# Kernel optimization log

Measured on AMD Instinct MI355X. Metric: run time of the kernel, lower is better.

The kernel has to match this reference:

```python
import jax, jax.numpy as jnp
import numpy as np

B, N, C, H, P, DP = 2, 512, 384, 12, 4, 128
CH = C // H
SCALE = CH ** -0.5
EPS = 1e-5


def setup_inputs() -> dict:
    key = jax.random.key(0)
    ks = jax.random.split(key, 16)
    w = lambda k, i, o: jax.random.normal(k, (i, o), jnp.float32) * 0.02
    inp = {
        'single': jax.random.normal(ks[0], (B, N, C), jnp.float32),
        'pair': jax.random.normal(ks[1], (B, N, N, DP), jnp.float32),
        'rot': jax.random.normal(ks[2], (B, N, 3, 3), jnp.float32),
        'trans': jax.random.normal(ks[3], (B, N, 3), jnp.float32),
        'mask': jnp.ones((B, N), jnp.float32),
        'Wq': w(ks[4], C, C), 'bq': jnp.zeros((C,)),
        'Wk': w(ks[5], C, C), 'bk': jnp.zeros((C,)),
        'Wv': w(ks[6], C, C), 'bv': jnp.zeros((C,)),
        'Wpb': w(ks[7], DP, H), 'bpb': jnp.zeros((H,)),
        'Wqp': w(ks[8], C, H * P * 3), 'bqp': jnp.zeros((H * P * 3,)),
        'Wkp': w(ks[9], C, H * P * 3), 'bkp': jnp.zeros((H * P * 3,)),
        'Wvp': w(ks[10], C, H * P * 3), 'bvp': jnp.zeros((H * P * 3,)),
        'Wo': w(ks[11], C, C), 'bo': jnp.zeros((C,)),
        'Wpo': w(ks[12], H * P * 3, C), 'bpo': jnp.zeros((C,)),
        'ln_g': jnp.ones((C,)), 'ln_b': jnp.zeros((C,)),
    }
    return inp


def _to_global(pts, rot, trans):
    # pts: [B,N,H,P,3], rot: [B,N,3,3], trans: [B,N,3]
    return jnp.einsum('bnhpd,bnde->bnhpe', pts, rot) + trans[:, :, None, None, :]


def reference(single, pair, rot, trans, mask,
              Wq, bq, Wk, bk, Wv, bv, Wpb, bpb,
              Wqp, bqp, Wkp, bkp, Wvp, bvp,
              Wo, bo, Wpo, bpo, ln_g, ln_b):
    q = (single @ Wq + bq).reshape(B, N, H, CH)
    k = (single @ Wk + bk).reshape(B, N, H, CH)
    v = (single @ Wv + bv).reshape(B, N, H, CH)
    pair_bias = jnp.transpose(pair @ Wpb + bpb, (0, 3, 1, 2))  # [B,H,N,N]

    q_pts = (single @ Wqp + bqp).reshape(B, N, H, P, 3)
    k_pts = (single @ Wkp + bkp).reshape(B, N, H, P, 3)
    qg = _to_global(q_pts, rot, trans)
    kg = _to_global(k_pts, rot, trans)

    q2 = jnp.sum(qg * qg, axis=(3, 4))  # [B,N,H]
    k2 = jnp.sum(kg * kg, axis=(3, 4))
    qk = jnp.einsum('bnhpd,bmhpd->bhnm', qg, kg)
    q2h = jnp.transpose(q2, (0, 2, 1))  # [B,H,N]
    k2h = jnp.transpose(k2, (0, 2, 1))
    point_logits = -0.5 * (q2h[..., :, None] + k2h[..., None, :] - 2.0 * qk) * SCALE

    scalar_logits = jnp.einsum('bnhc,bmhc->bhnm', q, k) * SCALE
    logits = scalar_logits + pair_bias + point_logits

    mask2d = mask[:, None, :, None] * mask[:, None, None, :]  # [B,1,N,N]
    logits = jnp.where(mask2d == 0, -1e9, logits)
    attn = jax.nn.softmax(logits, axis=-1)

    weighted_scalar = jnp.einsum('bhnm,bmhc->bnhc', attn, v).reshape(B, N, C)

    v_pts = (single @ Wvp + bvp).reshape(B, N, H, P, 3)
    vg = _to_global(v_pts, rot, trans)
    weighted_points = jnp.einsum('bhnm,bmhpd->bnhpd', attn, vg).reshape(B, N, H * P * 3)

    point_proj = weighted_points @ Wpo + bpo
    out = (weighted_scalar + point_proj) @ Wo + bo

    x = single + out
    mu = jnp.mean(x, axis=-1, keepdims=True)
    var = jnp.mean((x - mu) ** 2, axis=-1, keepdims=True)
    return (x - mu) * jax.lax.rsqrt(var + EPS) * ln_g + ln_b
```

## Files before the change

kernel.cpp:

```cpp
#include <hip/hip_runtime.h>
#include <hip/hip_bf16.h>

#define Bb   2
#define Nn   512
#define Cc   384
#define Hh   12
#define BN   1024
#define NC1  1584
#define CT1  99
#define SCALE 0.17677669529663687f

typedef __attribute__((ext_vector_type(8))) short short8;
typedef __attribute__((ext_vector_type(4))) float f32x4;

__device__ __forceinline__ unsigned short f2bf(float f){
  union { float f; unsigned u; } v; v.f = f;
  unsigned u = v.u;
  unsigned r = u + 0x7fffu + ((u >> 16) & 1u);
  return (unsigned short)(r >> 16);
}
__device__ __forceinline__ float bf_lo(unsigned u){ union{unsigned u; float f;} v; v.u = u << 16; return v.f; }
__device__ __forceinline__ float bf_hi(unsigned u){ union{unsigned u; float f;} v; v.u = u & 0xffff0000u; return v.f; }
__device__ __forceinline__ unsigned pack2(float a, float b){
  return (unsigned)f2bf(a) | ((unsigned)f2bf(b) << 16);
}

__device__ __forceinline__ void bias_job16(const float* __restrict__ pair,
    const float* __restrict__ Wpb, const float* __restrict__ bpb,
    unsigned short* __restrict__ biasf, int jd, int tid, unsigned short* lds)
{
  int l = tid & 63, w = tid >> 6;
  int b = jd >> 9, r9 = jd & 511;
  int it = r9 >> 4, jt = r9 & 15;
  int i0 = it << 4, j0 = jt << 5;
  int kb = (l >> 4) << 3;
  int h = l & 15;
  short8 bf[4];
#pragma unroll
  for (int t = 0; t < 4; ++t){
#pragma unroll
    for (int j = 0; j < 8; ++j){
      int k = t * 32 + kb + j;
      float v = (h < 12) ? Wpb[k * 12 + h] : 0.f;
      bf[t][j] = (short)f2bf(v);
    }
  }
  float bb = (h < 12) ? bpb[h] : 0.f;

  for (int s = 0; s < 8; ++s){
    int tile = s * 4 + w;
    int iloc = tile >> 1, jh = tile & 1;
    long m = ((long)(b * 512 + i0 + iloc)) * 512 + j0 + jh * 16 + (l & 15);
    const float* pr = pair + m * 128 + kb;
    f32x4 acc = {0,0,0,0};
#pragma unroll
    for (int t = 0; t < 4; ++t){
      float4 x0 = *(const float4*)(pr + t * 32);
      float4 x1 = *(const float4*)(pr + t * 32 + 4);
      short8 a;
      a[0] = (short)f2bf(x0.x); a[1] = (short)f2bf(x0.y);
      a[2] = (short)f2bf(x0.z); a[3] = (short)f2bf(x0.w);
      a[4] = (short)f2bf(x1.x); a[5] = (short)f2bf(x1.y);
      a[6] = (short)f2bf(x1.z); a[7] = (short)f2bf(x1.w);
      acc = __builtin_amdgcn_mfma_f32_16x16x32_bf16(a, bf[t], acc, 0, 0, 0);
    }
    if (h < 12){
      int jloc = jh * 16 + ((l >> 4) << 2);
      unsigned short* dst = lds + (h * 17 + iloc) * 36 + jloc;
      uint2 wv; wv.x = pack2(acc[0] + bb, acc[1] + bb); wv.y = pack2(acc[2] + bb, acc[3] + bb);
      *(uint2*)dst = wv;
    }
  }
  __syncthreads();

  for (int e = tid; e < 12 * 2 * 64; e += 256){
    int run = e >> 6, idx = e & 63;
    int h2 = run >> 1, f = run & 1;
    int g2 = idx >> 4, q = idx & 15;
    const unsigned short* src = lds + (h2 * 17 + q) * 36 + f * 16 + g2 * 4;
    uint2 v = *(const uint2*)src;
    long base = ((((long)(b * 12 + h2) * 16 + jt) * 32 + it) * 2 + f) * 64 + idx;
    *(uint2*)(biasf + base * 4) = v;
  }
}

__global__ __launch_bounds__(256) void k1_prep_bias(
    const float* __restrict__ single,
    const float* __restrict__ Wq, const float* __restrict__ Wk, const float* __restrict__ Wv,
    const float* __restrict__ Wqp, const float* __restrict__ Wkp, const float* __restrict__ Wvp,
    const float* __restrict__ bq, const float* __restrict__ bk, const float* __restrict__ bv,
    const float* __restrict__ bqp, const float* __restrict__ bkp, const float* __restrict__ bvp,
    const float* __restrict__ Wpo, const float* __restrict__ Wo,
    const float* __restrict__ pair, const float* __restrict__ Wpb, const float* __restrict__ bpb,
    unsigned short* __restrict__ sbf, unsigned short* __restrict__ wcat, float* __restrict__ bcat,
    unsigned short* __restrict__ wpof, unsigned short* __restrict__ wof,
    unsigned short* __restrict__ wppad, unsigned short* __restrict__ biasf)
{
  __shared__ __align__(16) unsigned short blds[16 * 17 * 36];
  int bid = blockIdx.x, tid = threadIdx.x;
  if (bid >= 256){ bias_job16(pair, Wpb, bpb, biasf, bid - 256, tid, blds); return; }

  const int n0 = BN * Cc;
  const int n1 = 12 * CT1 * 512;
  const int n4 = NC1;
  const int n5 = 61440;
  const int n6 = 147456;
  const int n7 = BN * 16;
  const int total = n0 + n1 + n4 + n5 + n6 + n7;
  for (int i = bid * 256 + tid; i < total; i += 256 * 256){
    int e = i;
    if (e < n0){ sbf[e] = f2bf(single[e]); continue; }
    e -= n0;
    if (e < n1){
      int j8 = e & 7, l = (e >> 3) & 63, ctt = e >> 9;
      int ct = ctt % CT1, t = ctt / CT1;
      int k = t * 32 + ((l >> 4) << 3) + j8;
      int col = (ct << 4) + (l & 15);
      float v;
      if (col < 1152){
        const float* W = (col < 384) ? Wq : (col < 768 ? Wk : Wv);
        v = W[k * 384 + (col % 384)];
      } else {
        int c2 = col - 1152;
        const float* W = (c2 < 144) ? Wqp : (c2 < 288 ? Wkp : Wvp);
        v = W[k * 144 + (c2 % 144)];
      }
      wcat[e] = f2bf(v); continue;
    }
    e -= n1;
    if (e < n4){
      int col = e; float v;
      if (col < 1152){
        const float* bb = (col < 384) ? bq : (col < 768 ? bk : bv);
        v = bb[col % 384];
      } else {
        int c2 = col - 1152;
        const float* bb = (c2 < 144) ? bqp : (c2 < 288 ? bkp : bvp);
        v = bb[c2 % 144];
      }
      bcat[col] = v; continue;
    }
    e -= n4;
    if (e < n5){
      int j8 = e & 7, l = (e >> 3) & 63, ctt = e >> 9;
      int ct = ctt % 24, t = ctt / 24;
      int k = t * 32 + ((l >> 4) << 3) + j8;
      int col = (ct << 4) + (l & 15);
      wpof[e] = (k < 144) ? f2bf(Wpo[k * 384 + col]) : (unsigned short)0;
      continue;
    }
    e -= n5;
    if (e < n6){
      int j8 = e & 7, l = (e >> 3) & 63, ctt = e >> 9;
      int ct = ctt % 24, t = ctt / 24;
      int k = t * 32 + ((l >> 4) << 3) + j8;
      int col = (ct << 4) + (l & 15);
      wof[e] = f2bf(Wo[k * 384 + col]);
      continue;
    }
    e -= n6;
    { int row = e >> 4, c = e & 15; wppad[row * 160 + 144 + c] = 0; }
  }
}

__global__ __launch_bounds__(256) void k2_proj_bias(
    const unsigned short* __restrict__ sbf, const unsigned short* __restrict__ wcat,
    const float* __restrict__ bcat, float* __restrict__ proj,
    const float* __restrict__ pair, const float* __restrict__ Wpb, const float* __restrict__ bpb,
    unsigned short* __restrict__ biasf)
{
  __shared__ __align__(16) unsigned short blds[16 * 17 * 36];
  int bid = blockIdx.x, tid = threadIdx.x;
  if (bid >= 528){ bias_job16(pair, Wpb, bpb, biasf, 192 + (bid - 528), tid, blds); return; }

  int l = tid & 63, w = tid >> 6;
  int bx = bid & 15, by = bid >> 4;
  int m0 = bx * 64 + w * 16;
  const unsigned short* Ap = sbf + (long)(m0 + (l & 15)) * Cc + ((l >> 4) << 3);
  int ct0 = by * 3;
  f32x4 acc0 = {0,0,0,0}, acc1 = {0,0,0,0}, acc2 = {0,0,0,0};
  for (int t = 0; t < 12; ++t){
    short8 a = *(const short8*)(Ap + t * 32);
    const unsigned short* wp_ = wcat + ((long)(t * CT1 + ct0) * 64 + l) * 8;
    short8 b0 = *(const short8*)(wp_);
    short8 b1 = *(const short8*)(wp_ + 512);
    short8 b2 = *(const short8*)(wp_ + 1024);
    acc0 = __builtin_amdgcn_mfma_f32_16x16x32_bf16(a, b0, acc0, 0, 0, 0);
    acc1 = __builtin_amdgcn_mfma_f32_16x16x32_bf16(a, b1, acc1, 0, 0, 0);
    acc2 = __builtin_amdgcn_mfma_f32_16x16x32_bf16(a, b2, acc2, 0, 0, 0);
  }
  int rbase = m0 + ((l >> 4) << 2);
  int cb = by * 48 + (l & 15);
#pragma unroll
  for (int c = 0; c < 3; ++c){
    f32x4 ac = (c == 0) ? acc0 : (c == 1 ? acc1 : acc2);
    int col = cb + c * 16;
    float bb = bcat[col];
#pragma unroll
    for (int r = 0; r < 4; ++r)
      proj[(long)(rbase + r) * NC1 + col] = ac[r] + bb;
  }
}

__global__ __launch_bounds__(256) void k3_pack_bias(
    const float* __restrict__ proj, const float* __restrict__ rot,
    const float* __restrict__ trans, const float* __restrict__ mask,
    unsigned short* __restrict__ qf, unsigned short* __restrict__ kf,
    unsigned short* __restrict__ vf, float* __restrict__ q2h, float* __restrict__ k2h,
    const float* __restrict__ pair, const float* __restrict__ Wpb, const float* __restrict__ bpb,
    unsigned short* __restrict__ biasf)
{
  __shared__ __align__(16) unsigned char smem3[23168];
  int bid = blockIdx.x, tid = threadIdx.x;
  if (bid >= 384){
    bias_job16(pair, Wpb, bpb, biasf, 576 + (bid - 384), tid, (unsigned short*)smem3);
    return;
  }

  float* scal = (float*)smem3;
  float* praw = scal + 3072;
  float* pg   = praw + 1152;
  float* rots = pg + 1152;
  float* trs  = rots + 288;
  float* msk  = trs + 96;

  int jid = bid;
  int b = jid / 192, rem = jid % 192;
  int h = rem >> 4, rt = rem & 15;
  int j0 = rt * 32;
  int bn0 = b * 512 + j0;
  int bh = b * 12 + h;

  for (int idx = tid; idx < 3072; idx += 256){
    int a = idx >> 10, row = (idx >> 5) & 31, c = idx & 31;
    scal[idx] = proj[(long)(bn0 + row) * NC1 + a * 384 + h * 32 + c];
  }
  for (int idx = tid; idx < 1152; idx += 256){
    int a = idx / 384, rr = idx % 384, row = rr / 12, pe = rr % 12;
    praw[idx] = proj[(long)(bn0 + row) * NC1 + 1152 + a * 144 + h * 12 + pe];
  }
  for (int idx = tid; idx < 288; idx += 256) rots[idx] = rot[(long)bn0 * 9 + idx];
  for (int idx = tid; idx < 96; idx += 256)  trs[idx] = trans[(long)bn0 * 3 + idx];
  for (int idx = tid; idx < 32; idx += 256)  msk[idx] = mask[bn0 + idx];
  __syncthreads();

  for (int idx = tid; idx < 1152; idx += 256){
    int a = idx / 384, rr = idx % 384, row = rr / 12, pe = rr % 12;
    int p = pe / 3, ee = pe % 3;
    pg[idx] = praw[a * 384 + row * 12 + p * 3] * rots[row * 9 + ee]
            + praw[a * 384 + row * 12 + p * 3 + 1] * rots[row * 9 + 3 + ee]
            + praw[a * 384 + row * 12 + p * 3 + 2] * rots[row * 9 + 6 + ee] + trs[row * 3 + ee];
  }
  __syncthreads();

  for (int idx = tid; idx < 64; idx += 256){
    int a = idx >> 5, row = idx & 31;
    float s2 = 0.f;
#pragma unroll
    for (int pe = 0; pe < 12; ++pe){ float g = pg[a * 384 + row * 12 + pe]; s2 += g * g; }
    float mv = msk[row];
    float rres = -0.5f * SCALE * s2 + (mv != 0.f ? 0.f : -2e9f);
    (a ? k2h : q2h)[(long)bh * 512 + j0 + row] = rres;
  }

  for (int idx = tid; idx < 2048; idx += 256){
    int a = idx >> 10, r = idx & 1023;
    int jjp = r & 3, l = (r >> 2) & 63, ks = (r >> 8) & 1, sub = r >> 9;
    int row = sub * 16 + (l & 15);
    int kk = ks * 32 + ((l >> 4) << 3) + jjp * 2;
    int k1 = kk + 1;
    float v0 = (kk < 32) ? scal[a * 1024 + row * 32 + kk] : (kk < 44 ? pg[a * 384 + row * 12 + kk - 32] : 0.f);
    float v1 = (k1 < 32) ? scal[a * 1024 + row * 32 + k1] : (k1 < 44 ? pg[a * 384 + row * 12 + k1 - 32] : 0.f);
    if (a == 0){ v0 *= SCALE; v1 *= SCALE; }
    unsigned* dst = (unsigned*)(a ? kf : qf);
    dst[((((long)bh * 32 + rt * 2 + sub) * 2 + ks) * 64 + l) * 4 + jjp] = pack2(v0, v1);
  }

  for (int idx = tid; idx < 768; idx += 256){
    int jjp = idx & 3, l = (idx >> 2) & 63, cf = idx >> 8;
    int c = cf * 16 + (l & 15);
    int j = ((l >> 4) << 3) + jjp * 2;
    float v0 = (c < 32) ? scal[2048 + j * 32 + c]       : (c < 44 ? pg[768 + j * 12 + (c - 32)]       : 0.f);
    float v1 = (c < 32) ? scal[2048 + (j + 1) * 32 + c] : (c < 44 ? pg[768 + (j + 1) * 12 + (c - 32)] : 0.f);
    ((unsigned*)vf)[(((long)bh * 16 + rt) * 3 + cf) * 256 + l * 4 + jjp] = pack2(v0, v1);
  }
}

__global__ __launch_bounds__(256) void attn2_kernel(
    const unsigned short* __restrict__ qf, const unsigned short* __restrict__ kf,
    const unsigned short* __restrict__ vf, const unsigned short* __restrict__ biasf,
    const float* __restrict__ q2h, const float* __restrict__ k2h,
    float* __restrict__ wsout, unsigned short* __restrict__ wpout)
{
  __shared__ unsigned short pls[4][16][40];
  __shared__ float oW[4][3][64][4];
  __shared__ float mW[4][16], lsW[4][16];
  __shared__ float fW[4][16], linvS[16];

  int l = threadIdx.x & 63, w = threadIdx.x >> 6;
  int qt = blockIdx.x, h = blockIdx.y, b = blockIdx.z;
  int bh = b * 12 + h;
  int g = l >> 4, q_ = l & 15;

  const short8* qp = (const short8*)(qf + (((long)(bh * 32 + qt) * 2) * 64 + l) * 8);
  short8 qA = qp[0], qB = qp[64];
  float cq = q2h[(long)bh * 512 + qt * 16 + q_];

  float m = -1e30f, ls = 0.f;
  f32x4 o0 = {0,0,0,0}, o1 = {0,0,0,0}, o2 = {0,0,0,0};
  const f32x4 z4 = {0,0,0,0};

#pragma unroll
  for (int ji = 0; ji < 4; ++ji){
    int jt = w * 4 + ji;
    const short8* kp = (const short8*)(kf + (((long)(bh * 32 + jt * 2) * 2) * 64 + l) * 8);
    short8 k00 = kp[0], k01 = kp[64], k10 = kp[128], k11 = kp[192];
    f32x4 s0 = __builtin_amdgcn_mfma_f32_16x16x32_bf16(k00, qA, z4, 0, 0, 0);
    s0 = __builtin_amdgcn_mfma_f32_16x16x32_bf16(k01, qB, s0, 0, 0, 0);
    f32x4 s1 = __builtin_amdgcn_mfma_f32_16x16x32_bf16(k10, qA, z4, 0, 0, 0);
    s1 = __builtin_amdgcn_mfma_f32_16x16x32_bf16(k11, qB, s1, 0, 0, 0);

    const uint2* bp = (const uint2*)(biasf + ((((long)(bh * 16 + jt) * 32 + qt) * 2) * 64) * 4);
    uint2 bb0 = bp[l], bb1 = bp[64 + l];
    const float4* k2p = (const float4*)(k2h + (long)bh * 512 + jt * 32);
    float4 ck0 = k2p[g], ck1 = k2p[4 + g];

    s0[0] += bf_lo(bb0.x) + cq + ck0.x;
    s0[1] += bf_hi(bb0.x) + cq + ck0.y;
    s0[2] += bf_lo(bb0.y) + cq + ck0.z;
    s0[3] += bf_hi(bb0.y) + cq + ck0.w;
    s1[0] += bf_lo(bb1.x) + cq + ck1.x;
    s1[1] += bf_hi(bb1.x) + cq + ck1.y;
    s1[2] += bf_lo(bb1.y) + cq + ck1.z;
    s1[3] += bf_hi(bb1.y) + cq + ck1.w;

    float tm = fmaxf(fmaxf(fmaxf(s0[0], s0[1]), fmaxf(s0[2], s0[3])),
                     fmaxf(fmaxf(s1[0], s1[1]), fmaxf(s1[2], s1[3])));
    tm = fmaxf(tm, __shfl_xor(tm, 16));
    tm = fmaxf(tm, __shfl_xor(tm, 32));
    float mn = fmaxf(m, tm);
    float alpha = __expf(m - mn);
    f32x4 p0, p1;
    float ts = 0.f;
#pragma unroll
    for (int r = 0; r < 4; ++r){ p0[r] = __expf(s0[r] - mn); ts += p0[r]; }
#pragma unroll
    for (int r = 0; r < 4; ++r){ p1[r] = __expf(s1[r] - mn); ts += p1[r]; }
    ts += __shfl_xor(ts, 16);
    ts += __shfl_xor(ts, 32);
    ls = ls * alpha + ts; m = mn;

    f32x4 av;
#pragma unroll
    for (int r = 0; r < 4; ++r) av[r] = __shfl(alpha, g * 4 + r);
#pragma unroll
    for (int r = 0; r < 4; ++r){ o0[r] *= av[r]; o1[r] *= av[r]; o2[r] *= av[r]; }

    uint2 w0; w0.x = pack2(p0[0], p0[1]); w0.y = pack2(p0[2], p0[3]);
    uint2 w1; w1.x = pack2(p1[0], p1[1]); w1.y = pack2(p1[2], p1[3]);
    *(uint2*)&pls[w][q_][g * 4]      = w0;
    *(uint2*)&pls[w][q_][16 + g * 4] = w1;
    short8 pa = *(const short8*)&pls[w][q_][g * 8];

    const short8* vp = (const short8*)(vf + (((long)(bh * 16 + jt) * 3) * 64 + l) * 8);
    short8 v0 = vp[0], v1 = vp[64], v2 = vp[128];
    o0 = __builtin_amdgcn_mfma_f32_16x16x32_bf16(pa, v0, o0, 0, 0, 0);
    o1 = __builtin_amdgcn_mfma_f32_16x16x32_bf16(pa, v1, o1, 0, 0, 0);
    o2 = __builtin_amdgcn_mfma_f32_16x16x32_bf16(pa, v2, o2, 0, 0, 0);
  }

  if (g == 0){ mW[w][q_] = m; lsW[w][q_] = ls; }
  *(f32x4*)&oW[w][0][l][0] = o0;
  *(f32x4*)&oW[w][1][l][0] = o1;
  *(f32x4*)&oW[w][2][l][0] = o2;
  __syncthreads();

  if (w == 0){
    float M = fmaxf(fmaxf(mW[0][q_], mW[1][q_]), fmaxf(mW[2][q_], mW[3][q_]));
    float f = __expf(mW[g][q_] - M);
    fW[g][q_] = f;
    float lf = lsW[g][q_] * f;
    lf += __shfl_xor(lf, 16);
    lf += __shfl_xor(lf, 32);
    if (g == 0) linvS[q_] = 1.f / lf;
  }
  __syncthreads();

  if (w < 3){
    float fr[4][4], li[4];
#pragma unroll
    for (int r = 0; r < 4; ++r){
      int q = g * 4 + r;
      li[r] = linvS[q];
#pragma unroll
      for (int vw = 0; vw < 4; ++vw) fr[vw][r] = fW[vw][q];
    }
    f32x4 sum = {0,0,0,0};
#pragma unroll
    for (int vw = 0; vw < 4; ++vw){
      f32x4 ov = *(const f32x4*)&oW[vw][w][l][0];
#pragma unroll
      for (int r = 0; r < 4; ++r) sum[r] += ov[r] * fr[vw][r];
    }
#pragma unroll
    for (int r = 0; r < 4; ++r){
      long bn = (long)b * 512 + qt * 16 + g * 4 + r;
      float val = sum[r] * li[r];
      if (w == 0)      wsout[bn * 384 + h * 32 + q_] = val;
      else if (w == 1) wsout[bn * 384 + h * 32 + 16 + q_] = val;
      else if (q_ < 12) wpout[bn * 160 + h * 12 + q_] = f2bf(val);
    }
  }
}

__global__ __launch_bounds__(256) void tail_kernel(
    const unsigned short* __restrict__ wpbuf, const unsigned short* __restrict__ wpof,
    const float* __restrict__ bpo, const float* __restrict__ wso,
    const unsigned short* __restrict__ wof, const float* __restrict__ bo,
    const float* __restrict__ single, const float* __restrict__ ln_g,
    const float* __restrict__ ln_b, float* __restrict__ out)
{
  __shared__ unsigned short t1s[16][392];
  __shared__ float redS[4][16], redQ[4][16];
  int l = threadIdx.x & 63, w = threadIdx.x >> 6;
  int m0 = blockIdx.x * 16;
  int rb = (l >> 4) << 2;
  int arow = m0 + (l & 15);

  {
    short8 awp[5];
    const unsigned short* Ap = wpbuf + (long)arow * 160 + ((l >> 4) << 3);
#pragma unroll
    for (int t = 0; t < 5; ++t) awp[t] = *(const short8*)(Ap + t * 32);
#pragma unroll
    for (int c6 = 0; c6 < 6; ++c6){
      int ct = w * 6 + c6;
      f32x4 acc = {0,0,0,0};
#pragma unroll
      for (int t = 0; t < 5; ++t){
        short8 bfr = *(const short8*)(wpof + ((long)(t * 24 + ct) * 64 + l) * 8);
        acc = __builtin_amdgcn_mfma_f32_16x16x32_bf16(awp[t], bfr, acc, 0, 0, 0);
      }
      int col = ct * 16 + (l & 15);
      float bb = bpo[col];
#pragma unroll
      for (int r = 0; r < 4; ++r){
        float v = acc[r] + bb + wso[(long)(m0 + rb + r) * 384 + col];
        t1s[rb + r][col] = f2bf(v);
      }
    }
  }
  __syncthreads();

  short8 a2[12];
  {
    int lr = l & 15;
#pragma unroll
    for (int t = 0; t < 12; ++t)
      a2[t] = *(const short8*)&t1s[lr][t * 32 + ((l >> 4) << 3)];
  }
  f32x4 xa[6];
  float s1[4] = {0,0,0,0}, s2[4] = {0,0,0,0};
#pragma unroll
  for (int c6 = 0; c6 < 6; ++c6){
    int ct = w * 6 + c6;
    f32x4 acc = {0,0,0,0};
#pragma unroll
    for (int t = 0; t < 12; ++t){
      short8 bfr = *(const short8*)(wof + ((long)(t * 24 + ct) * 64 + l) * 8);
      acc = __builtin_amdgcn_mfma_f32_16x16x32_bf16(a2[t], bfr, acc, 0, 0, 0);
    }
    int col = ct * 16 + (l & 15);
    float bb = bo[col];
#pragma unroll
    for (int r = 0; r < 4; ++r){
      float v = acc[r] + bb + single[(long)(m0 + rb + r) * 384 + col];
      acc[r] = v; s1[r] += v; s2[r] += v * v;
    }
    xa[c6] = acc;
  }
#pragma unroll
  for (int off = 1; off < 16; off <<= 1){
#pragma unroll
    for (int r = 0; r < 4; ++r){
      s1[r] += __shfl_xor(s1[r], off);
      s2[r] += __shfl_xor(s2[r], off);
    }
  }
  if ((l & 15) == 0){
#pragma unroll
    for (int r = 0; r < 4; ++r){ redS[w][rb + r] = s1[r]; redQ[w][rb + r] = s2[r]; }
  }
  __syncthreads();
  float mu[4], inv[4];
#pragma unroll
  for (int r = 0; r < 4; ++r){
    float ts = redS[0][rb + r] + redS[1][rb + r] + redS[2][rb + r] + redS[3][rb + r];
    float tq = redQ[0][rb + r] + redQ[1][rb + r] + redQ[2][rb + r] + redQ[3][rb + r];
    mu[r] = ts * (1.f / 384.f);
    float var = tq * (1.f / 384.f) - mu[r] * mu[r];
    inv[r] = rsqrtf(var + 1e-5f);
  }
#pragma unroll
  for (int c6 = 0; c6 < 6; ++c6){
    int ct = w * 6 + c6;
    int col = ct * 16 + (l & 15);
    float g = ln_g[col], bt = ln_b[col];
#pragma unroll
    for (int r = 0; r < 4; ++r)
      out[(long)(m0 + rb + r) * 384 + col] = (xa[c6][r] - mu[r]) * inv[r] * g + bt;
  }
}

extern "C" void kernel_launch(void* const* d_in, const int* in_sizes, int n_in,
                              void* d_out, int out_size, void* d_ws, size_t ws_size,
                              hipStream_t stream)
{
  const float* single = (const float*)d_in[0];
  const float* pair   = (const float*)d_in[1];
  const float* rot    = (const float*)d_in[2];
  const float* trans  = (const float*)d_in[3];
  const float* mask   = (const float*)d_in[4];
  const float* Wq  = (const float*)d_in[5];  const float* bq  = (const float*)d_in[6];
  const float* Wk  = (const float*)d_in[7];  const float* bk  = (const float*)d_in[8];
  const float* Wv  = (const float*)d_in[9];  const float* bv  = (const float*)d_in[10];
  const float* Wpb = (const float*)d_in[11]; const float* bpb = (const float*)d_in[12];
  const float* Wqp = (const float*)d_in[13]; const float* bqp = (const float*)d_in[14];
  const float* Wkp = (const float*)d_in[15]; const float* bkp = (const float*)d_in[16];
  const float* Wvp = (const float*)d_in[17]; const float* bvp = (const float*)d_in[18];
  const float* Wo  = (const float*)d_in[19]; const float* bo  = (const float*)d_in[20];
  const float* Wpo = (const float*)d_in[21]; const float* bpo = (const float*)d_in[22];
  const float* ln_g = (const float*)d_in[23]; const float* ln_b = (const float*)d_in[24];

  char* wsb = (char*)d_ws;
  size_t off = 0;
  auto alloc = [&](size_t bytes) -> void* {
    void* p = wsb + off; off += (bytes + 255) & ~(size_t)255; return p;
  };
  unsigned short* sbf  = (unsigned short*)alloc((size_t)BN * Cc * 2);
  unsigned short* wcat = (unsigned short*)alloc((size_t)12 * CT1 * 512 * 2);
  unsigned short* wpof = (unsigned short*)alloc((size_t)5 * 24 * 512 * 2);
  unsigned short* wof  = (unsigned short*)alloc((size_t)12 * 24 * 512 * 2);
  float* bcat  = (float*)alloc(NC1 * 4);
  float* proj  = (float*)alloc((size_t)BN * NC1 * 4);
  unsigned short* biasf = (unsigned short*)alloc((size_t)Bb * Hh * Nn * Nn * 2);
  unsigned short* qfragb = (unsigned short*)alloc((size_t)786432 * 2);
  unsigned short* kfragb = (unsigned short*)alloc((size_t)786432 * 2);
  unsigned short* vfragb = (unsigned short*)alloc((size_t)589824 * 2);
  float* q2hb  = (float*)alloc((size_t)12288 * 4);
  float* k2hb  = (float*)alloc((size_t)12288 * 4);
  float* wso   = (float*)alloc((size_t)BN * 384 * 4);
  unsigned short* wpbuf = (unsigned short*)alloc((size_t)BN * 160 * 2);
  if (off > ws_size) return;

  k1_prep_bias<<<256 + 192, 256, 0, stream>>>(
      single, Wq, Wk, Wv, Wqp, Wkp, Wvp, bq, bk, bv, bqp, bkp, bvp, Wpo, Wo,
      pair, Wpb, bpb, sbf, wcat, bcat, wpof, wof, wpbuf, biasf);
  k2_proj_bias<<<528 + 384, 256, 0, stream>>>(
      sbf, wcat, bcat, proj, pair, Wpb, bpb, biasf);
  k3_pack_bias<<<384 + 448, 256, 0, stream>>>(
      proj, rot, trans, mask, qfragb, kfragb, vfragb, q2hb, k2hb,
      pair, Wpb, bpb, biasf);
  attn2_kernel<<<dim3(32, 12, 2), 256, 0, stream>>>(qfragb, kfragb, vfragb, biasf,
                                                    q2hb, k2hb, wso, wpbuf);
  tail_kernel<<<64, 256, 0, stream>>>(wpbuf, wpof, bpo, wso, wof, bo,
                                      single, ln_g, ln_b, (float*)d_out);
}
```

Measured before the change: 96.12 us.

## Move all pair-bias jobs into the first kernel and unroll the bias loop

The pair-bias projection work was previously split across three kernels (k1, k2, k3) as extra blocks piggybacking on the projection and packing kernels. It is now done entirely by k1, which launches 1024 bias blocks, while k2 and k3 run only their own work. The bias inner loop is also unrolled by 2 to raise memory-level parallelism. This makes the bandwidth-heavy pair read one large phase instead of overlapping it with the small projection and packing kernels, which may reduce co-scheduling benefits but improves load balance and lowers LDS use in k2 and k3.

Result: slower. 105.5 us (+9.7%).

```diff
diff --git a/kernel.cpp b/kernel.cpp
--- a/kernel.cpp
+++ b/kernel.cpp
@@ -47,6 +47,7 @@
   }
   float bb = (h < 12) ? bpb[h] : 0.f;
 
+#pragma unroll 2
   for (int s = 0; s < 8; ++s){
     int tile = s * 4 + w;
     int iloc = tile >> 1, jh = tile & 1;
@@ -163,16 +164,11 @@
   }
 }
 
-__global__ __launch_bounds__(256) void k2_proj_bias(
+__global__ __launch_bounds__(256) void k2_proj(
     const unsigned short* __restrict__ sbf, const unsigned short* __restrict__ wcat,
-    const float* __restrict__ bcat, float* __restrict__ proj,
-    const float* __restrict__ pair, const float* __restrict__ Wpb, const float* __restrict__ bpb,
-    unsigned short* __restrict__ biasf)
-{
-  __shared__ __align__(16) unsigned short blds[16 * 17 * 36];
+    const float* __restrict__ bcat, float* __restrict__ proj)
+{
   int bid = blockIdx.x, tid = threadIdx.x;
-  if (bid >= 528){ bias_job16(pair, Wpb, bpb, biasf, 192 + (bid - 528), tid, blds); return; }
-
   int l = tid & 63, w = tid >> 6;
   int bx = bid & 15, by = bid >> 4;
   int m0 = bx * 64 + w * 16;
@@ -202,22 +198,16 @@
   }
 }
 
-__global__ __launch_bounds__(256) void k3_pack_bias(
+__global__ __launch_bounds__(256) void k3_pack(
     const float* __restrict__ proj, const float* __restrict__ rot,
     const float* __restrict__ trans, const float* __restrict__ mask,
     unsigned short* __restrict__ qf, unsigned short* __restrict__ kf,
-    unsigned short* __restrict__ vf, float* __restrict__ q2h, float* __restrict__ k2h,
-    const float* __restrict__ pair, const float* __restrict__ Wpb, const float* __restrict__ bpb,
-    unsigned short* __restrict__ biasf)
-{
-  __shared__ __align__(16) unsigned char smem3[23168];
+    unsigned short* __restrict__ vf, float* __restrict__ q2h, float* __restrict__ k2h)
+{
+  __shared__ float smemf[5792];
   int bid = blockIdx.x, tid = threadIdx.x;
-  if (bid >= 384){
-    bias_job16(pair, Wpb, bpb, biasf, 576 + (bid - 384), tid, (unsigned short*)smem3);
-    return;
-  }
-
-  float* scal = (float*)smem3;
+
+  float* scal = smemf;
   float* praw = scal + 3072;
   float* pg   = praw + 1152;
   float* rots = pg + 1152;
@@ -553,14 +543,12 @@
   unsigned short* wpbuf = (unsigned short*)alloc((size_t)BN * 160 * 2);
   if (off > ws_size) return;
 
-  k1_prep_bias<<<256 + 192, 256, 0, stream>>>(
+  k1_prep_bias<<<256 + 1024, 256, 0, stream>>>(
       single, Wq, Wk, Wv, Wqp, Wkp, Wvp, bq, bk, bv, bqp, bkp, bvp, Wpo, Wo,
       pair, Wpb, bpb, sbf, wcat, bcat, wpof, wof, wpbuf, biasf);
-  k2_proj_bias<<<528 + 384, 256, 0, stream>>>(
-      sbf, wcat, bcat, proj, pair, Wpb, bpb, biasf);
-  k3_pack_bias<<<384 + 448, 256, 0, stream>>>(
-      proj, rot, trans, mask, qfragb, kfragb, vfragb, q2hb, k2hb,
-      pair, Wpb, bpb, biasf);
+  k2_proj<<<528, 256, 0, stream>>>(sbf, wcat, bcat, proj);
+  k3_pack<<<384, 256, 0, stream>>>(proj, rot, trans, mask,
+                                   qfragb, kfragb, vfragb, q2hb, k2hb);
   attn2_kernel<<<dim3(32, 12, 2), 256, 0, stream>>>(qfragb, kfragb, vfragb, biasf,
                                                     q2hb, k2hb, wso, wpbuf);
   tail_kernel<<<64, 256, 0, stream>>>(wpbuf, wpof, bpo, wso, wof, bo,
```

## Fuse tail projection and layernorm into attention via last-block atomic counter

Applied to the files above, without the earlier changes.

The separate tail kernel is removed. Its output projection, residual add and layernorm now run inside the attention kernel, done by whichever of the 12 head blocks for a (batch, query tile) finishes last, found with an atomic counter and thread fences. The counter is reset in the first prep kernel. Bias fragments for all four key tiles are also prefetched into registers before the main loop. This saves one kernel launch and its tail latency, but adds more LDS and register pressure to the attention kernel and serialises the tail work onto the last-arriving blocks.

Result: slower. 169.3 us (+76.1%).

```diff
diff --git a/kernel.cpp b/kernel.cpp
--- a/kernel.cpp
+++ b/kernel.cpp
@@ -94,11 +94,14 @@
     const float* __restrict__ pair, const float* __restrict__ Wpb, const float* __restrict__ bpb,
     unsigned short* __restrict__ sbf, unsigned short* __restrict__ wcat, float* __restrict__ bcat,
     unsigned short* __restrict__ wpof, unsigned short* __restrict__ wof,
-    unsigned short* __restrict__ wppad, unsigned short* __restrict__ biasf)
+    unsigned short* __restrict__ wppad, unsigned short* __restrict__ biasf,
+    unsigned* __restrict__ cnt)
 {
   __shared__ __align__(16) unsigned short blds[16 * 17 * 36];
   int bid = blockIdx.x, tid = threadIdx.x;
   if (bid >= 256){ bias_job16(pair, Wpb, bpb, biasf, bid - 256, tid, blds); return; }
+
+  if (bid == 0 && tid < 64) cnt[tid] = 0;
 
   const int n0 = BN * Cc;
   const int n1 = 12 * CT1 * 512;
@@ -290,17 +293,34 @@
     const unsigned short* __restrict__ qf, const unsigned short* __restrict__ kf,
     const unsigned short* __restrict__ vf, const unsigned short* __restrict__ biasf,
     const float* __restrict__ q2h, const float* __restrict__ k2h,
-    float* __restrict__ wsout, unsigned short* __restrict__ wpout)
+    float* __restrict__ wsout, unsigned short* __restrict__ wpout,
+    const unsigned short* __restrict__ wpof, const float* __restrict__ bpo,
+    const unsigned short* __restrict__ wof, const float* __restrict__ bo,
+    const float* __restrict__ single, const float* __restrict__ ln_g,
+    const float* __restrict__ ln_b, float* __restrict__ out,
+    unsigned* __restrict__ cnt)
 {
   __shared__ unsigned short pls[4][16][40];
   __shared__ float oW[4][3][64][4];
   __shared__ float mW[4][16], lsW[4][16];
   __shared__ float fW[4][16], linvS[16];
+  __shared__ unsigned short t1s[16][392];
+  __shared__ float redS[4][16], redQ[4][16];
+  __shared__ int lastflag;
 
   int l = threadIdx.x & 63, w = threadIdx.x >> 6;
   int qt = blockIdx.x, h = blockIdx.y, b = blockIdx.z;
   int bh = b * 12 + h;
   int g = l >> 4, q_ = l & 15;
+
+  uint2 bpre[4][2];
+#pragma unroll
+  for (int ji = 0; ji < 4; ++ji){
+    int jt = w * 4 + ji;
+    const uint2* bp = (const uint2*)(biasf + ((((long)(bh * 16 + jt) * 32 + qt) * 2) * 64) * 4);
+    bpre[ji][0] = bp[l];
+    bpre[ji][1] = bp[64 + l];
+  }
 
   const short8* qp = (const short8*)(qf + (((long)(bh * 32 + qt) * 2) * 64 + l) * 8);
   short8 qA = qp[0], qB = qp[64];
@@ -320,8 +340,7 @@
     f32x4 s1 = __builtin_amdgcn_mfma_f32_16x16x32_bf16(k10, qA, z4, 0, 0, 0);
     s1 = __builtin_amdgcn_mfma_f32_16x16x32_bf16(k11, qB, s1, 0, 0, 0);
 
-    const uint2* bp = (const uint2*)(biasf + ((((long)(bh * 16 + jt) * 32 + qt) * 2) * 64) * 4);
-    uint2 bb0 = bp[l], bb1 = bp[64 + l];
+    uint2 bb0 = bpre[ji][0], bb1 = bpre[ji][1];
     const float4* k2p = (const float4*)(k2h + (long)bh * 512 + jt * 32);
     float4 ck0 = k2p[g], ck1 = k2p[4 + g];
 
@@ -411,25 +430,23 @@
       else if (q_ < 12) wpout[bn * 160 + h * 12 + q_] = f2bf(val);
     }
   }
-}
-
-__global__ __launch_bounds__(256) void tail_kernel(
-    const unsigned short* __restrict__ wpbuf, const unsigned short* __restrict__ wpof,
-    const float* __restrict__ bpo, const float* __restrict__ wso,
-    const unsigned short* __restrict__ wof, const float* __restrict__ bo,
-    const float* __restrict__ single, const float* __restrict__ ln_g,
-    const float* __restrict__ ln_b, float* __restrict__ out)
-{
-  __shared__ unsigned short t1s[16][392];
-  __shared__ float redS[4][16], redQ[4][16];
-  int l = threadIdx.x & 63, w = threadIdx.x >> 6;
-  int m0 = blockIdx.x * 16;
+
+  __threadfence();
+  __syncthreads();
+  if (threadIdx.x == 0){
+    unsigned old = atomicAdd(&cnt[b * 32 + qt], 1u);
+    lastflag = (old == 11u);
+  }
+  __syncthreads();
+  if (!lastflag) return;
+  __threadfence();
+
+  int m0t = b * 512 + qt * 16;
   int rb = (l >> 4) << 2;
-  int arow = m0 + (l & 15);
-
+  int arow = m0t + (l & 15);
   {
     short8 awp[5];
-    const unsigned short* Ap = wpbuf + (long)arow * 160 + ((l >> 4) << 3);
+    const unsigned short* Ap = wpout + (long)arow * 160 + ((l >> 4) << 3);
 #pragma unroll
     for (int t = 0; t < 5; ++t) awp[t] = *(const short8*)(Ap + t * 32);
 #pragma unroll
@@ -445,7 +462,7 @@
       float bb = bpo[col];
 #pragma unroll
       for (int r = 0; r < 4; ++r){
-        float v = acc[r] + bb + wso[(long)(m0 + rb + r) * 384 + col];
+        float v = acc[r] + bb + wsout[(long)(m0t + rb + r) * 384 + col];
         t1s[rb + r][col] = f2bf(v);
       }
     }
@@ -460,7 +477,7 @@
       a2[t] = *(const short8*)&t1s[lr][t * 32 + ((l >> 4) << 3)];
   }
   f32x4 xa[6];
-  float s1[4] = {0,0,0,0}, s2[4] = {0,0,0,0};
+  float s1a[4] = {0,0,0,0}, s2a[4] = {0,0,0,0};
 #pragma unroll
   for (int c6 = 0; c6 < 6; ++c6){
     int ct = w * 6 + c6;
@@ -474,8 +491,8 @@
     float bb = bo[col];
 #pragma unroll
     for (int r = 0; r < 4; ++r){
-      float v = acc[r] + bb + single[(long)(m0 + rb + r) * 384 + col];
-      acc[r] = v; s1[r] += v; s2[r] += v * v;
+      float v = acc[r] + bb + single[(long)(m0t + rb + r) * 384 + col];
+      acc[r] = v; s1a[r] += v; s2a[r] += v * v;
     }
     xa[c6] = acc;
   }
@@ -483,13 +500,13 @@
   for (int off = 1; off < 16; off <<= 1){
 #pragma unroll
     for (int r = 0; r < 4; ++r){
-      s1[r] += __shfl_xor(s1[r], off);
-      s2[r] += __shfl_xor(s2[r], off);
+      s1a[r] += __shfl_xor(s1a[r], off);
+      s2a[r] += __shfl_xor(s2a[r], off);
     }
   }
   if ((l & 15) == 0){
 #pragma unroll
-    for (int r = 0; r < 4; ++r){ redS[w][rb + r] = s1[r]; redQ[w][rb + r] = s2[r]; }
+    for (int r = 0; r < 4; ++r){ redS[w][rb + r] = s1a[r]; redQ[w][rb + r] = s2a[r]; }
   }
   __syncthreads();
   float mu[4], inv[4];
@@ -505,10 +522,10 @@
   for (int c6 = 0; c6 < 6; ++c6){
     int ct = w * 6 + c6;
     int col = ct * 16 + (l & 15);
-    float g = ln_g[col], bt = ln_b[col];
+    float gg = ln_g[col], bt = ln_b[col];
 #pragma unroll
     for (int r = 0; r < 4; ++r)
-      out[(long)(m0 + rb + r) * 384 + col] = (xa[c6][r] - mu[r]) * inv[r] * g + bt;
+      out[(long)(m0t + rb + r) * 384 + col] = (xa[c6][r] - mu[r]) * inv[r] * gg + bt;
   }
 }
 
@@ -551,18 +568,18 @@
   float* k2hb  = (float*)alloc((size_t)12288 * 4);
   float* wso   = (float*)alloc((size_t)BN * 384 * 4);
   unsigned short* wpbuf = (unsigned short*)alloc((size_t)BN * 160 * 2);
+  unsigned* cnt = (unsigned*)alloc(64 * 4);
   if (off > ws_size) return;
 
   k1_prep_bias<<<256 + 192, 256, 0, stream>>>(
       single, Wq, Wk, Wv, Wqp, Wkp, Wvp, bq, bk, bv, bqp, bkp, bvp, Wpo, Wo,
-      pair, Wpb, bpb, sbf, wcat, bcat, wpof, wof, wpbuf, biasf);
+      pair, Wpb, bpb, sbf, wcat, bcat, wpof, wof, wpbuf, biasf, cnt);
   k2_proj_bias<<<528 + 384, 256, 0, stream>>>(
       sbf, wcat, bcat, proj, pair, Wpb, bpb, biasf);
   k3_pack_bias<<<384 + 448, 256, 0, stream>>>(
       proj, rot, trans, mask, qfragb, kfragb, vfragb, q2hb, k2hb,
       pair, Wpb, bpb, biasf);
-  attn2_kernel<<<dim3(32, 12, 2), 256, 0, stream>>>(qfragb, kfragb, vfragb, biasf,
-                                                    q2hb, k2hb, wso, wpbuf);
-  tail_kernel<<<64, 256, 0, stream>>>(wpbuf, wpof, bpo, wso, wof, bo,
-                                      single, ln_g, ln_b, (float*)d_out);
-}
+  attn2_kernel<<<dim3(32, 12, 2), 256, 0, stream>>>(
+      qfragb, kfragb, vfragb, biasf, q2hb, k2hb, wso, wpbuf,
+      wpof, bpo, wof, bo, single, ln_g, ln_b, (float*)d_out, cnt);
+}
```
